# Kernel tuning notes

Hardware: AMD Instinct MI355X
Metric: run time of the kernel (lower is better)

## Reference

```python
import jax, jax.numpy as jnp
import numpy as np

N_E = 8192      # codebook size
E_DIM = 256     # codebook dim
BETA = 0.25

def setup_inputs() -> dict:
    key = jax.random.key(0)
    k1, k2 = jax.random.split(key)
    z = jax.random.normal(k1, (4, E_DIM, 16, 16, 16), dtype=jnp.float32)
    weight = jax.random.normal(k2, (N_E, E_DIM), dtype=jnp.float32)
    return {"z": z, "weight": weight}

def reference(z, weight):
    # b c d h w -> b d h w c
    z_t = jnp.transpose(z, (0, 2, 3, 4, 1))
    zf = z_t.reshape(-1, E_DIM)                          # [N, e_dim]
    # l2 pairwise distances: |z|^2 + |w|^2 - 2 z.w^T
    d = (jnp.sum(zf * zf, axis=1, keepdims=True)
         + jnp.sum(weight * weight, axis=1)
         - 2.0 * jnp.einsum('bd,nd->bn', zf, weight))    # [N, n_e]
    idx = jnp.argmin(d, axis=1)                          # [N]
    z_q = weight[idx].reshape(z_t.shape)                 # gather lookup
    # perplexity from cluster assignment histogram (avoids dense one-hot)
    counts = jax.ops.segment_sum(jnp.ones_like(idx, dtype=z.dtype), idx,
                                 num_segments=N_E)
    avg_probs = counts / zf.shape[0]
    perplexity = jnp.exp(-jnp.sum(avg_probs * jnp.log(avg_probs + 1e-10)))
    # commitment loss (z_q detached)
    loss = BETA * jnp.mean((jax.lax.stop_gradient(z_q) - z_t) ** 2)
    # straight-through estimator
    z_q_st = z_t + jax.lax.stop_gradient(z_q - z_t)
    out = jnp.transpose(z_q_st, (0, 4, 1, 2, 3))         # b d h w c -> b c d h w
    return out, loss, perplexity, idx
```

## Files before the change

### kernel.cpp

```cpp
#include <hip/hip_runtime.h>
#include <stdint.h>


#define M_TOTAL 16384
#define N_CODES 8192
#define KDIM    256
#define SPATIAL 4096
#define NSPLIT  8
#define CODES_PER_SPLIT  1024
#define CHUNK_CODES      32
#define CHUNKS_PER_SPLIT 32
#define CHUNK_HALFS      8192
#define CHUNK_BYTES      16384
#define SCORE_C          256.0f

typedef _Float16 v8hf __attribute__((ext_vector_type(8)));
typedef _Float16 v4hf __attribute__((ext_vector_type(4)));
typedef float    v4f  __attribute__((ext_vector_type(4)));

__global__ void prep_w_kernel(const float* __restrict__ w,
                              _Float16* __restrict__ wpk,
                              float* __restrict__ wsqC,
                              int* __restrict__ counts,
                              float* __restrict__ loss_acc) {
    int n = blockIdx.x;
    int lane = threadIdx.x;
    v4f v = ((const v4f*)(w + (size_t)n * KDIM))[lane];
    v4hf hv;
    float s = 0.0f;
#pragma unroll
    for (int j = 0; j < 4; j++) {
        float f = v[j];
        s += f * f;
        hv[j] = (_Float16)f;
    }
    const int d = lane * 4;
    const int g = d >> 3;
    const int sub = d & 7;
    size_t off = (size_t)(n >> 5) * CHUNK_HALFS
               + (size_t)(n & 31) * 256
               + ((g ^ (n & 7)) << 3) + sub;
    *(v4hf*)(wpk + off) = hv;
#pragma unroll
    for (int o = 32; o >= 1; o >>= 1) s += __shfl_xor(s, o);
    if (lane == 0) {
        wsqC[n] = s + SCORE_C;
        counts[n] = 0;
        if (n == 0) *loss_acc = 0.0f;
    }
}

__device__ __forceinline__ void top2u_merge(uint32_t& v1, int& i1, uint32_t& v2, int& i2,
                                            uint32_t o1, int oi1, uint32_t o2, int oi2) {
    bool ob = (o1 < v1) || (o1 == v1 && oi1 < i1);
    uint32_t n1v, n2v; int n1i, n2i;
    if (ob) {
        bool t = (v1 < o2) || (v1 == o2 && i1 < oi2);
        n1v = o1; n1i = oi1;
        n2v = t ? v1 : o2; n2i = t ? i1 : oi2;
    } else {
        bool t = (o1 < v2) || (o1 == v2 && oi1 < i2);
        n1v = v1; n1i = i1;
        n2v = t ? o1 : v2; n2i = t ? oi1 : i2;
    }
    v1 = n1v; i1 = n1i; v2 = n2v; i2 = n2i;
}

__global__ __launch_bounds__(128, 2) void gemm_kernel(
    const float* __restrict__ z,
    const _Float16* __restrict__ wpk,
    const float* __restrict__ wsqC,
    int* __restrict__ candbuf)
{
    __shared__ __align__(16) _Float16 ldsb[2][CHUNK_HALFS];

    const int bid   = blockIdx.x;
    const int split = bid & 7;
    const int rb    = bid >> 3;
    const int i0    = rb * 128;
    const int b     = i0 >> 12;
    const int s0    = i0 & (SPATIAL - 1);
    const int tid   = threadIdx.x;
    const int wave  = tid >> 6;
    const int lane  = tid & 63;
    const int r     = lane & 15;
    const int q     = lane >> 4;

    const char* wb = (const char*)wpk + (size_t)split * (CODES_PER_SPLIT * KDIM * 2);
    auto stage = [&](int chunk, int buf) {
        const char* gb = wb + (size_t)chunk * CHUNK_BYTES + wave * 8192 + lane * 16;
        _Float16* lb = &ldsb[buf][wave * 4096];
#pragma unroll
        for (int j = 0; j < 8; j++) {
            __builtin_amdgcn_global_load_lds(
                (const __attribute__((address_space(1))) void*)(gb + j * 1024),
                (__attribute__((address_space(3))) void*)(lb + j * 512), 16, 0, 0);
        }
    };
    stage(0, 0);

    v8hf a[4][8];
    {
        const float* zb = z + ((size_t)b << 20) + (size_t)(s0 + wave * 64 + r);
#pragma unroll
        for (int mt = 0; mt < 4; mt++) {
#pragma unroll
            for (int ks = 0; ks < 8; ks++) {
                const int kbase = ks * 32 + q * 8;
#pragma unroll
                for (int j = 0; j < 8; j++)
                    a[mt][ks][j] = (_Float16)zb[((size_t)(kbase + j) << 12) + mt * 16];
            }
        }
    }

    uint32_t k1[4][4], k2[4][4];
#pragma unroll
    for (int mt = 0; mt < 4; mt++)
#pragma unroll
    for (int g = 0; g < 4; g++) { k1[mt][g] = 0xFFFFFFFFu; k2[mt][g] = 0xFFFFFFFFu; }

    const float* wsqS = wsqC + split * CODES_PER_SPLIT;
    const int swz = r & 7;

    for (int it = 0; it < CHUNKS_PER_SPLIT; it++) {
        const int buf = it & 1;
        __syncthreads();
        if (it + 1 < CHUNKS_PER_SPLIT) stage(it + 1, buf ^ 1);

        v4f acc[4][2];
#pragma unroll
        for (int mt = 0; mt < 4; mt++)
#pragma unroll
        for (int st = 0; st < 2; st++) acc[mt][st] = (v4f){0.f, 0.f, 0.f, 0.f};

        const _Float16* L = &ldsb[buf][0];
#pragma unroll
        for (int st = 0; st < 2; st++) {
            const int rowoff = (st * 16 + r) * 256;
#pragma unroll
            for (int ks = 0; ks < 8; ks++) {
                const int gran = ((ks << 2) | q) ^ swz;
                v8hf bh = *(const v8hf*)(L + rowoff + (gran << 3));
#pragma unroll
                for (int mt = 0; mt < 4; mt++)
                    acc[mt][st] = __builtin_amdgcn_mfma_f32_16x16x32_f16(a[mt][ks], bh, acc[mt][st], 0, 0, 0);
            }
        }

#pragma unroll
        for (int st = 0; st < 2; st++) {
            const float wn = wsqS[(it << 5) + st * 16 + r];
            const uint32_t tag = (uint32_t)((it << 1) | st);
#pragma unroll
            for (int mt = 0; mt < 4; mt++)
#pragma unroll
            for (int g = 0; g < 4; g++) {
                float s = __builtin_fmaf(-2.0f, acc[mt][st][g], wn);
                uint32_t key = (__float_as_uint(s) & 0xFFFFFFC0u) | tag;
                uint32_t o1 = k1[mt][g], o2 = k2[mt][g];
                uint32_t hi = key > o1 ? key : o1;
                k2[mt][g] = hi < o2 ? hi : o2;
                k1[mt][g] = key < o1 ? key : o1;
            }
        }
    }

    const int nbase = split * CODES_PER_SPLIT + r;
#pragma unroll
    for (int mt = 0; mt < 4; mt++) {
#pragma unroll
        for (int g = 0; g < 4; g++) {
            uint32_t K1 = k1[mt][g], K2 = k2[mt][g];
            int n1 = nbase + (int)((K1 & 63u) << 4);
            int n2 = nbase + (int)((K2 & 63u) << 4);
#pragma unroll
            for (int off = 1; off < 16; off <<= 1) {
                uint32_t o1 = __shfl_xor(K1, off);
                int     on1 = __shfl_xor(n1, off);
                uint32_t o2 = __shfl_xor(K2, off);
                int     on2 = __shfl_xor(n2, off);
                top2u_merge(K1, n1, K2, n2, o1, on1, o2, on2);
            }
            if (r == 0) {
                const int row = i0 + wave * 64 + mt * 16 + q * 4 + g;
                candbuf[(size_t)row * 16 + split * 2]     = n1;
                candbuf[(size_t)row * 16 + split * 2 + 1] = n2;
            }
        }
    }
}

__global__ __launch_bounds__(256) void finish_kernel(
    const float* __restrict__ z, const float* __restrict__ weight,
    const int* __restrict__ candbuf,
    int* __restrict__ counts, float* __restrict__ loss_acc,
    float* __restrict__ out, float* __restrict__ out_idx_f)
{
    __shared__ int s_cand[32][16];
    __shared__ int s_fi[32];
    __shared__ float s_w[32][257];
    __shared__ double s_loss[4];

    const int i0 = blockIdx.x * 32;
    const int b  = i0 >> 12;
    const int s0 = i0 & (SPATIAL - 1);
    const int t  = threadIdx.x;

    for (int e = t; e < 32 * 16; e += 256)
        s_cand[e >> 4][e & 15] = candbuf[(size_t)(i0 + (e >> 4)) * 16 + (e & 15)];
    __syncthreads();

    const int row = t >> 3, seg = t & 7;
    const size_t zbase = ((size_t)b << 20) + (size_t)(s0 + row);
    float zs[32];
#pragma unroll
    for (int j = 0; j < 32; j++) zs[j] = z[zbase + ((size_t)(seg * 32 + j) << 12)];

    double dmin = 1e300; int nmin = 0x7fffffff;
    for (int c = 0; c < 16; c++) {
        const int n = s_cand[row][c];
        const float* wr = weight + (size_t)n * KDIM + seg * 32;
        double d = 0.0;
#pragma unroll
        for (int j = 0; j < 32; j++) {
            double df = (double)zs[j] - (double)wr[j];
            d += df * df;
        }
#pragma unroll
        for (int o = 1; o < 8; o <<= 1) d += __shfl_xor(d, o);
        if (d < dmin || (d == dmin && n < nmin)) { dmin = d; nmin = n; }
    }

    double lsum = 0.0;
    if (seg == 0) {
        s_fi[row] = nmin;
        out_idx_f[i0 + row] = (float)nmin;
        atomicAdd(&counts[nmin], 1);
        lsum = dmin;
    }
#pragma unroll
    for (int o = 1; o < 64; o <<= 1) lsum += __shfl_xor(lsum, o);
    if ((t & 63) == 0) s_loss[t >> 6] = lsum;
    __syncthreads();
    if (t == 0) atomicAdd(loss_acc, (float)(s_loss[0] + s_loss[1] + s_loss[2] + s_loss[3]));

    for (int e = t; e < 32 * KDIM; e += 256) {
        int rr = e >> 8, c = e & 255;
        s_w[rr][c] = weight[(size_t)s_fi[rr] * KDIM + c];
    }
    __syncthreads();
    const int m = t & 31, c0 = t >> 5;
    const size_t obase = ((size_t)b << 20) + (size_t)(s0 + m);
    for (int c = c0; c < KDIM; c += 8)
        out[obase + ((size_t)c << 12)] = s_w[m][c];
}

__global__ void finalize_kernel(const int* __restrict__ counts,
                                const float* __restrict__ loss_acc,
                                float* __restrict__ out_scalars)
{
    const int t = threadIdx.x;
    double s = 0.0;
    for (int n = t; n < N_CODES; n += 256) {
        double p = (double)counts[n] / (double)M_TOTAL;
        s -= p * log(p + 1e-10);
    }
#pragma unroll
    for (int o = 32; o >= 1; o >>= 1) s += __shfl_xor(s, o);
    __shared__ double sds[4];
    if ((t & 63) == 0) sds[t >> 6] = s;
    __syncthreads();
    if (t == 0) {
        double tot = sds[0] + sds[1] + sds[2] + sds[3];
        out_scalars[0] = (float)(0.25 * (double)(*loss_acc) / (double)(M_TOTAL * KDIM));
        out_scalars[1] = (float)exp(tot);
    }
}

extern "C" void kernel_launch(void* const* d_in, const int* in_sizes, int n_in,
                              void* d_out, int out_size, void* d_ws, size_t ws_size,
                              hipStream_t stream) {
    const float* z      = (const float*)d_in[0];
    const float* weight = (const float*)d_in[1];
    float* out = (float*)d_out;

    size_t off = 0;
    auto carve = [&](size_t bytes) {
        void* p = (char*)d_ws + off;
        off += (bytes + 255) & ~(size_t)255;
        return p;
    };
    _Float16* wpk     = (_Float16*)carve((size_t)N_CODES * KDIM * 2);
    float*    wsqC    = (float*)   carve((size_t)N_CODES * 4);
    int*      candbuf = (int*)     carve((size_t)M_TOTAL * 16 * 4);
    int*      counts  = (int*)     carve((size_t)N_CODES * 4);
    float*    lossac  = (float*)   carve(16);

    float* out_scalars = out + (size_t)4 * KDIM * SPATIAL;
    float* out_idx_f   = out_scalars + 2;

    prep_w_kernel<<<dim3(N_CODES), dim3(64), 0, stream>>>(weight, wpk, wsqC, counts, lossac);
    gemm_kernel<<<dim3(128 * NSPLIT), dim3(128), 0, stream>>>(z, wpk, wsqC, candbuf);
    finish_kernel<<<dim3(M_TOTAL / 32), dim3(256), 0, stream>>>(
        z, weight, candbuf, counts, lossac, out, out_idx_f);
    finalize_kernel<<<dim3(1), dim3(256), 0, stream>>>(counts, lossac, out_scalars);
}
```

Baseline: 224.8 us.

## Restructure VQ argmin into single-wave pipelined GEMM with folded norms and pruned rescoring

The GEMM kernel becomes one wave per block with 16-code chunks. Each chunk carries its half-norm bias in the staged LDS buffer, so the accumulator starts from that bias and the search becomes a max with no separate norm load or fma. Staging uses two chunks of lookahead with explicit waitcnt in place of __syncthreads. Candidates now carry their approximate scores, which lets the finish kernel skip exact fp64 rescoring of candidates that fall outside a cutoff. z is staged through shared memory for coalesced reads, and loss accumulates in double. The risks are fp16 score precision against the fixed pruning margin, and the hand-tuned waitcnt correctness.

```diff
diff --git a/kernel.cpp b/kernel.cpp
--- a/kernel.cpp
+++ b/kernel.cpp
@@ -8,23 +8,26 @@
 #define SPATIAL 4096
 #define NSPLIT  8
 #define CODES_PER_SPLIT  1024
-#define CHUNK_CODES      32
-#define CHUNKS_PER_SPLIT 32
-#define CHUNK_HALFS      8192
-#define CHUNK_BYTES      16384
-#define SCORE_C          256.0f
+#define CHUNK_CODES      16
+#define CHUNKS_PER_SPLIT 64
+#define CHUNK_BYTES      9216
+#define CHUNK_HALFS      4608
 
 typedef _Float16 v8hf __attribute__((ext_vector_type(8)));
 typedef _Float16 v4hf __attribute__((ext_vector_type(4)));
 typedef float    v4f  __attribute__((ext_vector_type(4)));
 
-__global__ void prep_w_kernel(const float* __restrict__ w,
-                              _Float16* __restrict__ wpk,
-                              float* __restrict__ wsqC,
-                              int* __restrict__ counts,
-                              float* __restrict__ loss_acc) {
-    int n = blockIdx.x;
-    int lane = threadIdx.x;
+#define WAITCNT_VM9   0x0F79
+#define WAITCNT_VM0   0x0F70
+#define WAITCNT_LGKM0 0xC07F
+
+__global__ __launch_bounds__(256) void prep_w_kernel(
+    const float* __restrict__ w, _Float16* __restrict__ wpk,
+    int* __restrict__ counts, double* __restrict__ loss_acc)
+{
+    const int t = threadIdx.x;
+    const int n = blockIdx.x * 4 + (t >> 6);
+    const int lane = t & 63;
     v4f v = ((const v4f*)(w + (size_t)n * KDIM))[lane];
     v4hf hv;
     float s = 0.0f;
@@ -34,74 +37,73 @@
         s += f * f;
         hv[j] = (_Float16)f;
     }
-    const int d = lane * 4;
-    const int g = d >> 3;
-    const int sub = d & 7;
-    size_t off = (size_t)(n >> 5) * CHUNK_HALFS
-               + (size_t)(n & 31) * 256
-               + ((g ^ (n & 7)) << 3) + sub;
+    const int chunk = n >> 4;
+    const int row   = n & 15;
+    const int g     = lane >> 1;
+    const int gg    = g ^ (n & 7);
+    size_t off = (size_t)chunk * CHUNK_HALFS + row * 256 + gg * 8 + (lane & 1) * 4;
     *(v4hf*)(wpk + off) = hv;
 #pragma unroll
     for (int o = 32; o >= 1; o >>= 1) s += __shfl_xor(s, o);
     if (lane == 0) {
-        wsqC[n] = s + SCORE_C;
-        counts[n] = 0;
-        if (n == 0) *loss_acc = 0.0f;
-    }
-}
-
-__device__ __forceinline__ void top2u_merge(uint32_t& v1, int& i1, uint32_t& v2, int& i2,
-                                            uint32_t o1, int oi1, uint32_t o2, int oi2) {
-    bool ob = (o1 < v1) || (o1 == v1 && oi1 < i1);
+        float* hwp = (float*)((char*)wpk + (size_t)chunk * CHUNK_BYTES + 8192);
+        hwp[row] = 1024.0f - 0.5f * s;
+    }
+    const int gi = blockIdx.x * 256 + t;
+    if (gi < N_CODES) counts[gi] = 0;
+    if (gi == 0) *loss_acc = 0.0;
+}
+
+__device__ __forceinline__ void top2max_merge(uint32_t& v1, int& i1, uint32_t& v2, int& i2,
+                                              uint32_t o1, int oi1, uint32_t o2, int oi2) {
+    bool ob = (o1 > v1) || (o1 == v1 && oi1 < i1);
     uint32_t n1v, n2v; int n1i, n2i;
     if (ob) {
-        bool t = (v1 < o2) || (v1 == o2 && i1 < oi2);
+        bool t2 = (v1 > o2) || (v1 == o2 && i1 < oi2);
         n1v = o1; n1i = oi1;
-        n2v = t ? v1 : o2; n2i = t ? i1 : oi2;
+        n2v = t2 ? v1 : o2; n2i = t2 ? i1 : oi2;
     } else {
-        bool t = (o1 < v2) || (o1 == v2 && oi1 < i2);
+        bool t2 = (o1 > v2) || (o1 == v2 && oi1 < i2);
         n1v = v1; n1i = i1;
-        n2v = t ? o1 : v2; n2i = t ? oi1 : i2;
+        n2v = t2 ? o1 : v2; n2i = t2 ? oi1 : i2;
     }
     v1 = n1v; i1 = n1i; v2 = n2v; i2 = n2i;
 }
 
-__global__ __launch_bounds__(128, 2) void gemm_kernel(
+__global__ __launch_bounds__(64, 2) void gemm_kernel(
     const float* __restrict__ z,
     const _Float16* __restrict__ wpk,
-    const float* __restrict__ wsqC,
-    int* __restrict__ candbuf)
+    int4* __restrict__ candbuf)
 {
-    __shared__ __align__(16) _Float16 ldsb[2][CHUNK_HALFS];
+    __shared__ __align__(16) _Float16 lds[2][CHUNK_HALFS];
 
     const int bid   = blockIdx.x;
     const int split = bid & 7;
     const int rb    = bid >> 3;
-    const int i0    = rb * 128;
+    const int i0    = rb * 64;
     const int b     = i0 >> 12;
     const int s0    = i0 & (SPATIAL - 1);
-    const int tid   = threadIdx.x;
-    const int wave  = tid >> 6;
-    const int lane  = tid & 63;
+    const int lane  = threadIdx.x;
     const int r     = lane & 15;
     const int q     = lane >> 4;
 
-    const char* wb = (const char*)wpk + (size_t)split * (CODES_PER_SPLIT * KDIM * 2);
+    const char* wsplit = (const char*)wpk + (size_t)split * CHUNKS_PER_SPLIT * CHUNK_BYTES;
     auto stage = [&](int chunk, int buf) {
-        const char* gb = wb + (size_t)chunk * CHUNK_BYTES + wave * 8192 + lane * 16;
-        _Float16* lb = &ldsb[buf][wave * 4096];
-#pragma unroll
-        for (int j = 0; j < 8; j++) {
+        const char* gb = wsplit + (size_t)chunk * CHUNK_BYTES + lane * 16;
+        _Float16* lb = &lds[buf][lane * 8];
+#pragma unroll
+        for (int j = 0; j < 9; j++) {
             __builtin_amdgcn_global_load_lds(
                 (const __attribute__((address_space(1))) void*)(gb + j * 1024),
                 (__attribute__((address_space(3))) void*)(lb + j * 512), 16, 0, 0);
         }
     };
     stage(0, 0);
+    stage(1, 1);
 
     v8hf a[4][8];
     {
-        const float* zb = z + ((size_t)b << 20) + (size_t)(s0 + wave * 64 + r);
+        const float* zb = z + ((size_t)b << 20) + (size_t)(s0 + r);
 #pragma unroll
         for (int mt = 0; mt < 4; mt++) {
 #pragma unroll
@@ -118,74 +120,68 @@
 #pragma unroll
     for (int mt = 0; mt < 4; mt++)
 #pragma unroll
-    for (int g = 0; g < 4; g++) { k1[mt][g] = 0xFFFFFFFFu; k2[mt][g] = 0xFFFFFFFFu; }
-
-    const float* wsqS = wsqC + split * CODES_PER_SPLIT;
+    for (int g = 0; g < 4; g++) { k1[mt][g] = 0u; k2[mt][g] = 0u; }
+
     const int swz = r & 7;
 
-    for (int it = 0; it < CHUNKS_PER_SPLIT; it++) {
+    auto body = [&](int it, int buf) {
+        const float hwv = *(const float*)((const char*)&lds[buf][0] + 8192 + r * 4);
+        v4f acc[4];
+#pragma unroll
+        for (int mt = 0; mt < 4; mt++) acc[mt] = (v4f){hwv, hwv, hwv, hwv};
+
+        const _Float16* L = &lds[buf][0];
+#pragma unroll
+        for (int ks = 0; ks < 8; ks++) {
+            const int gran = ((ks << 2) | q) ^ swz;
+            v8hf bh = *(const v8hf*)(L + r * 256 + (gran << 3));
+#pragma unroll
+            for (int mt = 0; mt < 4; mt++)
+                acc[mt] = __builtin_amdgcn_mfma_f32_16x16x32_f16(a[mt][ks], bh, acc[mt], 0, 0, 0);
+        }
+        const uint32_t tag = (uint32_t)it;
+#pragma unroll
+        for (int mt = 0; mt < 4; mt++)
+#pragma unroll
+        for (int g = 0; g < 4; g++) {
+            uint32_t key = (__float_as_uint(acc[mt][g]) & 0xFFFFFFC0u) | tag;
+            uint32_t o1 = k1[mt][g], o2 = k2[mt][g];
+            uint32_t hi = key > o2 ? key : o2;
+            k2[mt][g] = hi < o1 ? hi : o1;
+            k1[mt][g] = key > o1 ? key : o1;
+        }
+    };
+
+#pragma unroll 1
+    for (int it = 0; it < CHUNKS_PER_SPLIT - 1; it++) {
         const int buf = it & 1;
-        __syncthreads();
-        if (it + 1 < CHUNKS_PER_SPLIT) stage(it + 1, buf ^ 1);
-
-        v4f acc[4][2];
-#pragma unroll
-        for (int mt = 0; mt < 4; mt++)
-#pragma unroll
-        for (int st = 0; st < 2; st++) acc[mt][st] = (v4f){0.f, 0.f, 0.f, 0.f};
-
-        const _Float16* L = &ldsb[buf][0];
-#pragma unroll
-        for (int st = 0; st < 2; st++) {
-            const int rowoff = (st * 16 + r) * 256;
-#pragma unroll
-            for (int ks = 0; ks < 8; ks++) {
-                const int gran = ((ks << 2) | q) ^ swz;
-                v8hf bh = *(const v8hf*)(L + rowoff + (gran << 3));
-#pragma unroll
-                for (int mt = 0; mt < 4; mt++)
-                    acc[mt][st] = __builtin_amdgcn_mfma_f32_16x16x32_f16(a[mt][ks], bh, acc[mt][st], 0, 0, 0);
-            }
-        }
-
-#pragma unroll
-        for (int st = 0; st < 2; st++) {
-            const float wn = wsqS[(it << 5) + st * 16 + r];
-            const uint32_t tag = (uint32_t)((it << 1) | st);
-#pragma unroll
-            for (int mt = 0; mt < 4; mt++)
-#pragma unroll
-            for (int g = 0; g < 4; g++) {
-                float s = __builtin_fmaf(-2.0f, acc[mt][st][g], wn);
-                uint32_t key = (__float_as_uint(s) & 0xFFFFFFC0u) | tag;
-                uint32_t o1 = k1[mt][g], o2 = k2[mt][g];
-                uint32_t hi = key > o1 ? key : o1;
-                k2[mt][g] = hi < o2 ? hi : o2;
-                k1[mt][g] = key < o1 ? key : o1;
-            }
-        }
-    }
-
-    const int nbase = split * CODES_PER_SPLIT + r;
+        __builtin_amdgcn_s_waitcnt(WAITCNT_VM9);
+        body(it, buf);
+        __builtin_amdgcn_s_waitcnt(WAITCNT_LGKM0);
+        if (it < CHUNKS_PER_SPLIT - 2) stage(it + 2, buf);
+    }
+    __builtin_amdgcn_s_waitcnt(WAITCNT_VM0);
+    body(CHUNKS_PER_SPLIT - 1, (CHUNKS_PER_SPLIT - 1) & 1);
+
+    const int nsbase = split * CODES_PER_SPLIT + r;
 #pragma unroll
     for (int mt = 0; mt < 4; mt++) {
 #pragma unroll
         for (int g = 0; g < 4; g++) {
             uint32_t K1 = k1[mt][g], K2 = k2[mt][g];
-            int n1 = nbase + (int)((K1 & 63u) << 4);
-            int n2 = nbase + (int)((K2 & 63u) << 4);
+            int n1 = nsbase + (int)((K1 & 63u) << 4);
+            int n2 = nsbase + (int)((K2 & 63u) << 4);
 #pragma unroll
             for (int off = 1; off < 16; off <<= 1) {
                 uint32_t o1 = __shfl_xor(K1, off);
                 int     on1 = __shfl_xor(n1, off);
                 uint32_t o2 = __shfl_xor(K2, off);
                 int     on2 = __shfl_xor(n2, off);
-                top2u_merge(K1, n1, K2, n2, o1, on1, o2, on2);
+                top2max_merge(K1, n1, K2, n2, o1, on1, o2, on2);
             }
             if (r == 0) {
-                const int row = i0 + wave * 64 + mt * 16 + q * 4 + g;
-                candbuf[(size_t)row * 16 + split * 2]     = n1;
-                candbuf[(size_t)row * 16 + split * 2 + 1] = n2;
+                const int row = i0 + mt * 16 + q * 4 + g;
+                candbuf[(size_t)row * 8 + split] = make_int4((int)K1, n1, (int)K2, n2);
             }
         }
     }
@@ -193,13 +189,13 @@
 
 __global__ __launch_bounds__(256) void finish_kernel(
     const float* __restrict__ z, const float* __restrict__ weight,
-    const int* __restrict__ candbuf,
-    int* __restrict__ counts, float* __restrict__ loss_acc,
+    const int4* __restrict__ candbuf,
+    int* __restrict__ counts, double* __restrict__ loss_acc,
     float* __restrict__ out, float* __restrict__ out_idx_f)
 {
-    __shared__ int s_cand[32][16];
-    __shared__ int s_fi[32];
-    __shared__ float s_w[32][257];
+    __shared__ int4  s_cand[32][8];
+    __shared__ float s_zw[32][KDIM + 1];
+    __shared__ int   s_fi[32];
     __shared__ double s_loss[4];
 
     const int i0 = blockIdx.x * 32;
@@ -207,19 +203,36 @@
     const int s0 = i0 & (SPATIAL - 1);
     const int t  = threadIdx.x;
 
-    for (int e = t; e < 32 * 16; e += 256)
-        s_cand[e >> 4][e & 15] = candbuf[(size_t)(i0 + (e >> 4)) * 16 + (e & 15)];
+    s_cand[t >> 3][t & 7] = candbuf[(size_t)(i0 + (t >> 3)) * 8 + (t & 7)];
+
+    for (int e = t; e < 32 * KDIM; e += 256) {
+        const int c = e >> 5, rr = e & 31;
+        s_zw[rr][c] = z[((size_t)b << 20) + ((size_t)c << 12) + s0 + rr];
+    }
     __syncthreads();
 
     const int row = t >> 3, seg = t & 7;
-    const size_t zbase = ((size_t)b << 20) + (size_t)(s0 + row);
     float zs[32];
 #pragma unroll
-    for (int j = 0; j < 32; j++) zs[j] = z[zbase + ((size_t)(seg * 32 + j) << 12)];
-
-    double dmin = 1e300; int nmin = 0x7fffffff;
+    for (int j = 0; j < 32; j++) zs[j] = s_zw[row][seg * 32 + j];
+
+    float da[16];
+    float dmin_a = 3.4e38f;
+#pragma unroll
+    for (int sp = 0; sp < 8; sp++) {
+        int4 c = s_cand[row][sp];
+        da[sp * 2]     = 2048.0f - 2.0f * __uint_as_float((uint32_t)c.x & 0xFFFFFFC0u);
+        da[sp * 2 + 1] = 2048.0f - 2.0f * __uint_as_float((uint32_t)c.z & 0xFFFFFFC0u);
+        dmin_a = fminf(dmin_a, fminf(da[sp * 2], da[sp * 2 + 1]));
+    }
+    const float cutoff = dmin_a + 0.5f;
+
+    double dbest = 1e300; int nbest = 0x7fffffff;
+#pragma unroll 1
     for (int c = 0; c < 16; c++) {
-        const int n = s_cand[row][c];
+        if (da[c] > cutoff) continue;
+        int4 cc = s_cand[row][c >> 1];
+        const int n = (c & 1) ? cc.w : cc.y;
         const float* wr = weight + (size_t)n * KDIM + seg * 32;
         double d = 0.0;
 #pragma unroll
@@ -229,35 +242,35 @@
         }
 #pragma unroll
         for (int o = 1; o < 8; o <<= 1) d += __shfl_xor(d, o);
-        if (d < dmin || (d == dmin && n < nmin)) { dmin = d; nmin = n; }
+        if (d < dbest || (d == dbest && n < nbest)) { dbest = d; nbest = n; }
     }
 
     double lsum = 0.0;
     if (seg == 0) {
-        s_fi[row] = nmin;
-        out_idx_f[i0 + row] = (float)nmin;
-        atomicAdd(&counts[nmin], 1);
-        lsum = dmin;
+        s_fi[row] = nbest;
+        out_idx_f[i0 + row] = (float)nbest;
+        atomicAdd(&counts[nbest], 1);
+        lsum = dbest;
     }
 #pragma unroll
     for (int o = 1; o < 64; o <<= 1) lsum += __shfl_xor(lsum, o);
     if ((t & 63) == 0) s_loss[t >> 6] = lsum;
     __syncthreads();
-    if (t == 0) atomicAdd(loss_acc, (float)(s_loss[0] + s_loss[1] + s_loss[2] + s_loss[3]));
+    if (t == 0) atomicAdd(loss_acc, s_loss[0] + s_loss[1] + s_loss[2] + s_loss[3]);
 
     for (int e = t; e < 32 * KDIM; e += 256) {
-        int rr = e >> 8, c = e & 255;
-        s_w[rr][c] = weight[(size_t)s_fi[rr] * KDIM + c];
+        const int rr = e >> 8, c = e & 255;
+        s_zw[rr][c] = weight[(size_t)s_fi[rr] * KDIM + c];
     }
     __syncthreads();
     const int m = t & 31, c0 = t >> 5;
     const size_t obase = ((size_t)b << 20) + (size_t)(s0 + m);
     for (int c = c0; c < KDIM; c += 8)
-        out[obase + ((size_t)c << 12)] = s_w[m][c];
+        out[obase + ((size_t)c << 12)] = s_zw[m][c];
 }
 
 __global__ void finalize_kernel(const int* __restrict__ counts,
-                                const float* __restrict__ loss_acc,
+                                const double* __restrict__ loss_acc,
                                 float* __restrict__ out_scalars)
 {
     const int t = threadIdx.x;
@@ -273,7 +286,7 @@
     __syncthreads();
     if (t == 0) {
         double tot = sds[0] + sds[1] + sds[2] + sds[3];
-        out_scalars[0] = (float)(0.25 * (double)(*loss_acc) / (double)(M_TOTAL * KDIM));
+        out_scalars[0] = (float)(0.25 * (*loss_acc) / (double)(M_TOTAL * KDIM));
         out_scalars[1] = (float)exp(tot);
     }
 }
@@ -291,17 +304,16 @@
         off += (bytes + 255) & ~(size_t)255;
         return p;
     };
-    _Float16* wpk     = (_Float16*)carve((size_t)N_CODES * KDIM * 2);
-    float*    wsqC    = (float*)   carve((size_t)N_CODES * 4);
-    int*      candbuf = (int*)     carve((size_t)M_TOTAL * 16 * 4);
+    _Float16* wpk     = (_Float16*)carve((size_t)(N_CODES / CHUNK_CODES) * CHUNK_BYTES);
+    int4*     candbuf = (int4*)    carve((size_t)M_TOTAL * 8 * 16);
     int*      counts  = (int*)     carve((size_t)N_CODES * 4);
-    float*    lossac  = (float*)   carve(16);
+    double*   lossac  = (double*)  carve(16);
 
     float* out_scalars = out + (size_t)4 * KDIM * SPATIAL;
     float* out_idx_f   = out_scalars + 2;
 
-    prep_w_kernel<<<dim3(N_CODES), dim3(64), 0, stream>>>(weight, wpk, wsqC, counts, lossac);
-    gemm_kernel<<<dim3(128 * NSPLIT), dim3(128), 0, stream>>>(z, wpk, wsqC, candbuf);
+    prep_w_kernel<<<dim3(N_CODES / 4), dim3(256), 0, stream>>>(weight, wpk, counts, lossac);
+    gemm_kernel<<<dim3(M_TOTAL / 64 * NSPLIT), dim3(64), 0, stream>>>(z, wpk, candbuf);
     finish_kernel<<<dim3(M_TOTAL / 32), dim3(256), 0, stream>>>(
         z, weight, candbuf, counts, lossac, out, out_idx_f);
     finalize_kernel<<<dim3(1), dim3(256), 0, stream>>>(counts, lossac, out_scalars);
```

New measurement: 209.8 us. -6.7%, faster.
